# Performance work log

Hardware: AMD Instinct MI355X
Metric: run time of the kernel (lower is better)

## Reference

```python
import jax, jax.numpy as jnp
import numpy as np

EPS = 0.3
LAYERS = 2


def setup_inputs() -> dict:
    key = jax.random.key(0)
    ks = jax.random.split(key, 8)
    N, F, H, C, E = 50000, 512, 128, 40, 800000

    def xavier(k, shape):
        fan_out, fan_in = shape[0], shape[-1]
        std = 1.414 * np.sqrt(2.0 / (fan_in + fan_out))
        return (jax.random.normal(k, shape, jnp.float32) * std).astype(jnp.float32)

    return {
        "x": jax.random.normal(ks[0], (N, F), jnp.float32),
        "t1_w": xavier(ks[1], (H, F)),
        "t1_b": jnp.zeros((H,), jnp.float32),
        "t2_w": xavier(ks[2], (C, H)),
        "t2_b": jnp.zeros((C,), jnp.float32),
        "gate_w": xavier(ks[3], (LAYERS, 2 * H)),  # Linear(2H,1) weight per layer
        "gate_b": jnp.zeros((LAYERS,), jnp.float32),
        "edge_index": jax.random.randint(ks[4], (2, E), 0, N, jnp.int32),
    }


def reference(x, t1_w, t1_b, t2_w, t2_b, gate_w, gate_b, edge_index):
    N = x.shape[0]
    H = t1_w.shape[0]
    row, col = edge_index[0], edge_index[1]  # source, target

    # norm_degree = degree(row).clamp(min=1) ** -0.5
    deg = jax.ops.segment_sum(jnp.ones_like(row, dtype=x.dtype), row, num_segments=N)
    nd = jnp.clip(deg, 1.0) ** -0.5  # [N]
    nd_r, nd_c = nd[row], nd[col]    # [E]

    # dropout is identity in eval mode
    h = jax.nn.relu(x @ t1_w.T + t1_b)  # [N,H]
    raw = h
    for l in range(LAYERS):
        h_src = h[row]  # x_j, [E,H]
        h_dst = h[col]  # [E,H]
        # gate(cat([h[row], h[col]])) == h_src @ W[:H] + h_dst @ W[H:] + b
        g = jnp.tanh(h_src @ gate_w[l, :H] + h_dst @ gate_w[l, H:] + gate_b[l])  # [E]
        norm = g * nd_r * nd_c  # [E]
        agg = jax.ops.segment_sum(norm[:, None] * h_src, col, num_segments=N)  # scatter-add at targets
        h = EPS * raw + agg
    out = h @ t2_w.T + t2_b  # [N,C]
    return jax.nn.log_softmax(out, axis=1)
```

## Files before the change

kernel.cpp:

```cpp
#include <hip/hip_runtime.h>
#include <math.h>

#define F_DIM 512
#define H_DIM 128
#define C_DIM 40
#define EPS_F 0.3f
#define NBLK 256

typedef float f32x4 __attribute__((ext_vector_type(4)));
typedef unsigned int u32x4 __attribute__((ext_vector_type(4)));
typedef __bf16 bf16x8 __attribute__((ext_vector_type(8)));
typedef unsigned short ushort_t;
typedef unsigned char uchar_t;

__device__ inline float bflo(unsigned t) { return __builtin_bit_cast(float, t << 16); }
__device__ inline float bfhi(unsigned t) { return __builtin_bit_cast(float, t & 0xffff0000u); }
__device__ inline unsigned short f2bf(float f) {
  unsigned u = __builtin_bit_cast(unsigned, f);
  u = (u + 0x7fffu + ((u >> 16) & 1u)) >> 16;
  return (unsigned short)u;
}
__device__ inline unsigned pack2bf(float a, float b) {
  unsigned ua = __builtin_bit_cast(unsigned, a);
  unsigned ub = __builtin_bit_cast(unsigned, b);
  ua = (ua + 0x7fffu + ((ua >> 16) & 1u)) >> 16;
  ub = (ub + 0x7fffu + ((ub >> 16) & 1u)) >> 16;
  return ua | (ub << 16);
}


__global__ __launch_bounds__(256) void part_count(const int* __restrict__ row,
    const int* __restrict__ col, int* __restrict__ blkhist, int E, int nbkt, int chunk) {
  __shared__ int ch[256], rh[256];
  int t = threadIdx.x, b = blockIdx.x;
  ch[t] = 0; rh[t] = 0;
  __syncthreads();
  int s = b * chunk, e = min(E, s + chunk);
  for (int i = s + t; i < e; i += 256) {
    atomicAdd(&ch[((unsigned)col[i]) >> 8], 1);
    atomicAdd(&rh[((unsigned)row[i]) >> 8], 1);
  }
  __syncthreads();
  if (t < nbkt) {
    blkhist[t * NBLK + b] = ch[t];
    blkhist[(nbkt + t) * NBLK + b] = rh[t];
  }
}

__global__ __launch_bounds__(256) void part_scatter(const int* __restrict__ row,
    const int* __restrict__ col, const int* __restrict__ blkhist,
    int* __restrict__ bktbase, unsigned* __restrict__ colpart,
    uchar_t* __restrict__ rowpart, int E, int nbkt, int chunk) {
  __shared__ int sbase[400];
  __shared__ int stot[400];
  __shared__ int psum[256];
  __shared__ int sc[400];
  __shared__ int coff[400];
  int t = threadIdx.x, b = blockIdx.x;
  int nrows = 2 * nbkt;
  for (int rr = t; rr < nrows; rr += 256) {
    const int* rp = &blkhist[rr * NBLK];
    int pre = 0, tot = 0;
    for (int i = 0; i < NBLK; ++i) {
      int v = rp[i];
      pre += (i < b) ? v : 0;
      tot += v;
    }
    sbase[rr] = pre; stot[rr] = tot;
  }
  __syncthreads();
  int e0 = (2 * t     < nrows) ? stot[2 * t]     : 0;
  int e1 = (2 * t + 1 < nrows) ? stot[2 * t + 1] : 0;
  psum[t] = e0 + e1;
  __syncthreads();
  for (int off = 1; off < 256; off <<= 1) {
    int add = (t >= off) ? psum[t - off] : 0;
    __syncthreads();
    psum[t] += add;
    __syncthreads();
  }
  int pex = (t == 0) ? 0 : psum[t - 1];
  if (2 * t < nrows)     sc[2 * t]     = pex + sbase[2 * t];
  if (2 * t + 1 < nrows) sc[2 * t + 1] = pex + e0 + sbase[2 * t + 1];
  if (b == 0) {
    if (2 * t < nrows)     bktbase[2 * t]     = pex;
    if (2 * t + 1 < nrows) bktbase[2 * t + 1] = pex + e0;
    if (t == 0) bktbase[nrows] = 2 * E;
  }
  for (int rr = t; rr < nrows; rr += 256) coff[rr] = 0;
  __syncthreads();
  int s = b * chunk, e = min(E, s + chunk);
  for (int i = s + t; i < e; i += 256) {
    unsigned c = (unsigned)col[i], r = (unsigned)row[i];
    int bc = (int)(c >> 8), br = (int)(r >> 8);
    int pc = sc[bc] + atomicAdd(&coff[bc], 1);
    colpart[pc] = (r << 8) | (c & 255u);
    int pr = sc[nbkt + br] + atomicAdd(&coff[nbkt + br], 1) - E;
    rowpart[pr] = (uchar_t)(r & 255u);
  }
}

__global__ __launch_bounds__(256) void bucket_both(const unsigned* __restrict__ colpart,
    const uchar_t* __restrict__ rowpart, const int* __restrict__ bktbase,
    int* __restrict__ col_ptr, int* __restrict__ csr_src, float* __restrict__ nd,
    int N, int E, int nbkt) {
  __shared__ int cnt[256], ex[256], off[256];
  int t = threadIdx.x, bb = blockIdx.x;
  if (bb < nbkt) {
    int bkt = bb;
    int s = bktbase[bkt], e = bktbase[bkt + 1];
    cnt[t] = 0; off[t] = 0;
    __syncthreads();
    for (int i = s + t; i < e; i += 256)
      atomicAdd(&cnt[(int)(colpart[i] & 255u)], 1);
    __syncthreads();
    ex[t] = cnt[t];
    __syncthreads();
    for (int o = 1; o < 256; o <<= 1) {
      int v = (t >= o) ? ex[t - o] : 0;
      __syncthreads();
      ex[t] += v;
      __syncthreads();
    }
    int excl = (t == 0) ? 0 : ex[t - 1];
    __syncthreads();
    ex[t] = excl;
    __syncthreads();
    int node = bkt * 256 + t;
    if (node < N) col_ptr[node] = s + ex[t];
    if (bkt == 0 && t == 0) col_ptr[N] = E;
    for (int i = s + t; i < e; i += 256) {
      unsigned p = colpart[i];
      int lb = (int)(p & 255u);
      int dst = s + ex[lb] + atomicAdd(&off[lb], 1);
      csr_src[dst] = (int)(p >> 8);
    }
  } else {
    int bkt = bb - nbkt;
    int s = bktbase[nbkt + bkt] - E, e = bktbase[nbkt + bkt + 1] - E;
    cnt[t] = 0;
    __syncthreads();
    for (int i = s + t; i < e; i += 256)
      atomicAdd(&cnt[(int)rowpart[i]], 1);
    __syncthreads();
    int node = bkt * 256 + t;
    if (node < N) {
      int d = cnt[t] < 1 ? 1 : cnt[t];
      nd[node] = 1.0f / sqrtf((float)d);
    }
  }
}


__global__ __launch_bounds__(256) void gemm1_mfma(const float* __restrict__ x,
    const float* __restrict__ w, const float* __restrict__ b,
    ushort_t* __restrict__ hbf, int N) {
  __shared__ u32x4 AsBuf[1024];
  __shared__ u32x4 BsBuf[1024];
  char* Asc = (char*)AsBuf;
  char* Bsc = (char*)BsBuf;

  int t = threadIdx.x;
  int lane = t & 63;
  int wid = t >> 6;
  int wm = wid >> 1;
  int wn = wid & 1;
  int m0 = blockIdx.x * 128;

  f32x4 acc[4][4];
#pragma unroll
  for (int i = 0; i < 4; ++i)
#pragma unroll
    for (int j = 0; j < 4; ++j) acc[i][j] = (f32x4){0.f, 0.f, 0.f, 0.f};

  float bias[4];
#pragma unroll
  for (int j = 0; j < 4; ++j) bias[j] = b[wn * 64 + j * 16 + (lane & 15)];

  for (int kk = 0; kk < F_DIM; kk += 64) {
#pragma unroll
    for (int q = 0; q < 4; ++q) {
      int c = q * 256 + t;
      int row = c >> 3, kc = c & 7;
      int gm = m0 + row;
      f32x4 v0 = {0.f, 0.f, 0.f, 0.f}, v1 = {0.f, 0.f, 0.f, 0.f};
      if (gm < N) {
        const float* src = &x[(size_t)gm * F_DIM + kk + kc * 8];
        v0 = *(const f32x4*)src;
        v1 = *(const f32x4*)(src + 4);
      }
      u32x4 pk;
      pk[0] = pack2bf(v0[0], v0[1]);
      pk[1] = pack2bf(v0[2], v0[3]);
      pk[2] = pack2bf(v1[0], v1[1]);
      pk[3] = pack2bf(v1[2], v1[3]);
      *(u32x4*)(Asc + row * 128 + ((kc ^ (row & 7)) << 4)) = pk;
    }
#pragma unroll
    for (int q = 0; q < 4; ++q) {
      int c = q * 256 + t;
      int row = c >> 3, kc = c & 7;
      const float* src = &w[(size_t)row * F_DIM + kk + kc * 8];
      f32x4 v0 = *(const f32x4*)src;
      f32x4 v1 = *(const f32x4*)(src + 4);
      u32x4 pk;
      pk[0] = pack2bf(v0[0], v0[1]);
      pk[1] = pack2bf(v0[2], v0[3]);
      pk[2] = pack2bf(v1[0], v1[1]);
      pk[3] = pack2bf(v1[2], v1[3]);
      *(u32x4*)(Bsc + row * 128 + ((kc ^ (row & 7)) << 4)) = pk;
    }
    __syncthreads();
#pragma unroll
    for (int kh = 0; kh < 2; ++kh) {
      bf16x8 af[4], bfr[4];
      int kc = kh * 4 + (lane >> 4);
#pragma unroll
      for (int i = 0; i < 4; ++i) {
        int row = wm * 64 + i * 16 + (lane & 15);
        af[i] = *(const bf16x8*)(Asc + row * 128 + ((kc ^ (row & 7)) << 4));
      }
#pragma unroll
      for (int j = 0; j < 4; ++j) {
        int row = wn * 64 + j * 16 + (lane & 15);
        bfr[j] = *(const bf16x8*)(Bsc + row * 128 + ((kc ^ (row & 7)) << 4));
      }
#pragma unroll
      for (int i = 0; i < 4; ++i)
#pragma unroll
        for (int j = 0; j < 4; ++j)
          acc[i][j] = __builtin_amdgcn_mfma_f32_16x16x32_bf16(af[i], bfr[j], acc[i][j], 0, 0, 0);
    }
    __syncthreads();
  }

#pragma unroll
  for (int i = 0; i < 4; ++i)
#pragma unroll
    for (int j = 0; j < 4; ++j) {
      int col = wn * 64 + j * 16 + (lane & 15);
      int rbase = m0 + wm * 64 + i * 16 + ((lane >> 4) * 4);
#pragma unroll
      for (int r = 0; r < 4; ++r) {
        int gr = rbase + r;
        if (gr < N) hbf[(size_t)gr * H_DIM + col] = f2bf(fmaxf(acc[i][j][r] + bias[j], 0.f));
      }
    }
}


__global__ __launch_bounds__(256) void gate_s(const ushort_t* __restrict__ hbf,
    const float* __restrict__ gwl, const float* __restrict__ gb, int layer,
    float* __restrict__ s1, float* __restrict__ s2, int N) {
  int wid = (blockIdx.x * 256 + threadIdx.x) >> 6;
  int lane = threadIdx.x & 63;
  if (wid >= N) return;
  unsigned tv = *(const unsigned*)&hbf[(size_t)wid * H_DIM + lane * 2];
  float hx = bflo(tv), hy = bfhi(tv);
  float2 g1 = *(const float2*)&gwl[lane * 2];
  float2 g2 = *(const float2*)&gwl[H_DIM + lane * 2];
  float p1 = hx * g1.x + hy * g1.y;
  float p2 = hx * g2.x + hy * g2.y;
  for (int off = 32; off > 0; off >>= 1) {
    p1 += __shfl_xor(p1, off);
    p2 += __shfl_xor(p2, off);
  }
  if (lane == 0) {
    s1[wid] = p1;
    s2[wid] = p2 + gb[layer];
  }
}


template <bool GATE>
__global__ __launch_bounds__(256) void agg_kernel(const ushort_t* __restrict__ hbf,
    const ushort_t* __restrict__ rawbf, const float* __restrict__ s1,
    const float* __restrict__ s2pb, const float* __restrict__ nd,
    const int* __restrict__ col_ptr, const int* __restrict__ csr_src,
    ushort_t* __restrict__ houtbf,
    const float* __restrict__ gwl, const float* __restrict__ gb, int layer,
    float* __restrict__ s1o, float* __restrict__ s2o, int N) {
  int wid = (blockIdx.x * 256 + threadIdx.x) >> 6;
  int lane = threadIdx.x & 63;
  if (wid >= N) return;
  int v = wid;
  int p0 = col_ptr[v], p1 = col_ptr[v + 1];
  float s2v = s2pb[v];
  float ndv = nd[v];
  float ax = 0.f, ay = 0.f;
  for (int base = p0; base < p1; base += 64) {
    int idx = base + lane;
    int u = 0;
    float cf = 0.f;
    if (idx < p1) {
      u = csr_src[idx];
      cf = tanhf(s1[u] + s2v) * nd[u] * ndv;
    }
    int cnt = p1 - base;
    if (cnt > 64) cnt = 64;
    int j = 0;
    for (; j + 4 <= cnt; j += 4) {
      int u0 = __shfl(u, j + 0), u1 = __shfl(u, j + 1);
      int u2 = __shfl(u, j + 2), u3 = __shfl(u, j + 3);
      float c0 = __shfl(cf, j + 0), c1 = __shfl(cf, j + 1);
      float c2 = __shfl(cf, j + 2), c3 = __shfl(cf, j + 3);
      unsigned t0 = *(const unsigned*)&hbf[(size_t)u0 * H_DIM + lane * 2];
      unsigned t1 = *(const unsigned*)&hbf[(size_t)u1 * H_DIM + lane * 2];
      unsigned t2 = *(const unsigned*)&hbf[(size_t)u2 * H_DIM + lane * 2];
      unsigned t3 = *(const unsigned*)&hbf[(size_t)u3 * H_DIM + lane * 2];
      ax += c0 * bflo(t0) + c1 * bflo(t1) + c2 * bflo(t2) + c3 * bflo(t3);
      ay += c0 * bfhi(t0) + c1 * bfhi(t1) + c2 * bfhi(t2) + c3 * bfhi(t3);
    }
    for (; j < cnt; ++j) {
      int uj = __shfl(u, j);
      float cj = __shfl(cf, j);
      unsigned tj = *(const unsigned*)&hbf[(size_t)uj * H_DIM + lane * 2];
      ax += cj * bflo(tj);
      ay += cj * bfhi(tj);
    }
  }
  unsigned rv = *(const unsigned*)&rawbf[(size_t)v * H_DIM + lane * 2];
  float ox = EPS_F * bflo(rv) + ax;
  float oy = EPS_F * bfhi(rv) + ay;
  *(unsigned*)&houtbf[(size_t)v * H_DIM + lane * 2] = pack2bf(ox, oy);
  if (GATE) {
    float2 g1 = *(const float2*)&gwl[lane * 2];
    float2 g2 = *(const float2*)&gwl[H_DIM + lane * 2];
    float q1 = ox * g1.x + oy * g1.y;
    float q2 = ox * g2.x + oy * g2.y;
    for (int off = 32; off > 0; off >>= 1) {
      q1 += __shfl_xor(q1, off);
      q2 += __shfl_xor(q2, off);
    }
    if (lane == 0) {
      s1o[v] = q1;
      s2o[v] = q2 + gb[layer];
    }
  }
}


__global__ __launch_bounds__(256) void gemm2_lsm(const ushort_t* __restrict__ hbf,
    const float* __restrict__ w, const float* __restrict__ b,
    float* __restrict__ out, int N) {
  __shared__ float ws[C_DIM][129];
  __shared__ float bsh[C_DIM];
  __shared__ float hsm[4][H_DIM];
  int t = threadIdx.x;
  for (int i = t; i < C_DIM * H_DIM; i += 256) ws[i / H_DIM][i % H_DIM] = w[i];
  if (t < C_DIM) bsh[t] = b[t];
  __syncthreads();
  int wave = t >> 6, lane = t & 63;
  for (int vb = blockIdx.x * 4; vb < N; vb += gridDim.x * 4) {
    int v = vb + wave;
    bool act = v < N;
    if (act) {
      unsigned hv = *(const unsigned*)&hbf[(size_t)v * H_DIM + lane * 2];
      hsm[wave][lane * 2] = bflo(hv);
      hsm[wave][lane * 2 + 1] = bfhi(hv);
    }
    __syncthreads();
    float acc = 0.f;
    if (act && lane < C_DIM) {
#pragma unroll 8
      for (int k = 0; k < H_DIM; ++k)
        acc = fmaf(hsm[wave][k], ws[lane][k], acc);
      acc += bsh[lane];
    }
    float m = (lane < C_DIM) ? acc : -1e30f;
    for (int off = 32; off > 0; off >>= 1) m = fmaxf(m, __shfl_xor(m, off));
    float ex = (lane < C_DIM) ? expf(acc - m) : 0.f;
    float s = ex;
    for (int off = 32; off > 0; off >>= 1) s += __shfl_xor(s, off);
    float lse = m + logf(s);
    if (act && lane < C_DIM) out[(size_t)v * C_DIM + lane] = acc - lse;
    __syncthreads();
  }
}


extern "C" void kernel_launch(void* const* d_in, const int* in_sizes, int n_in,
                              void* d_out, int out_size, void* d_ws, size_t ws_size,
                              hipStream_t stream) {
  const float* x   = (const float*)d_in[0];
  const float* t1w = (const float*)d_in[1];
  const float* t1b = (const float*)d_in[2];
  const float* t2w = (const float*)d_in[3];
  const float* t2b = (const float*)d_in[4];
  const float* gw  = (const float*)d_in[5];
  const float* gb  = (const float*)d_in[6];
  const int*   ei  = (const int*)d_in[7];
  const int N = in_sizes[0] / F_DIM;
  const int E = in_sizes[7] / 2;
  float* out = (float*)d_out;

  char* p = (char*)d_ws;
  auto take = [&](size_t bytes) {
    char* r = p;
    p += (bytes + 255) & ~(size_t)255;
    return r;
  };
  ushort_t* h0 = (ushort_t*)take((size_t)N * H_DIM * 2);
  ushort_t* h1 = (ushort_t*)take((size_t)N * H_DIM * 2);
  ushort_t* h2 = (ushort_t*)take((size_t)N * H_DIM * 2);
  float* s1a = (float*)take((size_t)N * 4);
  float* s2a = (float*)take((size_t)N * 4);
  float* s1b = (float*)take((size_t)N * 4);
  float* s2b = (float*)take((size_t)N * 4);
  float* nd  = (float*)take((size_t)N * 4);
  int* col_ptr = (int*)take((size_t)(N + 1) * 4);
  int* csr_src = (int*)take((size_t)E * 4);

  const int nbkt = (N + 255) >> 8;
  const int chunk = (E + NBLK - 1) / NBLK;

  int* blkhist = (int*)take((size_t)2 * nbkt * NBLK * 4);
  int* bktbase = (int*)take((size_t)(2 * nbkt + 1) * 4);
  unsigned* colpart = (unsigned*)take((size_t)E * 4);
  uchar_t* rowpart  = (uchar_t*)take((size_t)E);

  const int* row = ei;
  const int* col = ei + E;

  gemm1_mfma<<<(N + 127) / 128, 256, 0, stream>>>(x, t1w, t1b, h0, N);

  part_count<<<NBLK, 256, 0, stream>>>(row, col, blkhist, E, nbkt, chunk);
  part_scatter<<<NBLK, 256, 0, stream>>>(row, col, blkhist, bktbase, colpart, rowpart, E, nbkt, chunk);
  bucket_both<<<2 * nbkt, 256, 0, stream>>>(colpart, rowpart, bktbase, col_ptr, csr_src, nd, N, E, nbkt);

  int nwb = (N + 3) / 4;
  gate_s<<<nwb, 256, 0, stream>>>(h0, gw + 0 * 2 * H_DIM, gb, 0, s1a, s2a, N);
  agg_kernel<true><<<nwb, 256, 0, stream>>>(h0, h0, s1a, s2a, nd, col_ptr, csr_src, h1,
                                            gw + 1 * 2 * H_DIM, gb, 1, s1b, s2b, N);
  agg_kernel<false><<<nwb, 256, 0, stream>>>(h1, h0, s1b, s2b, nd, col_ptr, csr_src, h2,
                                             nullptr, nullptr, 0, nullptr, nullptr, N);

  gemm2_lsm<<<1024, 256, 0, stream>>>(h2, t2w, t2b, out, N);
}
```

Baseline: 210.8 us.

## Fuse gate projection into GEMM1 and final GEMM/log-softmax into last aggregation

Computes the layer-0 gate dot products in the GEMM1 epilogue via cross-lane and shared-memory reductions, which removes the separate gate_s kernel and a reread of h0. The last aggregation now also does the output projection and log-softmax, so the h2 round trip and the gemm2 launch go away. Gate scores and the node degree norm are packed into one float2 per node to cut scattered gathers. The gather loop reads 16-byte chunks with four edges per wave iteration. In exchange, the final kernel loads the full output weight matrix into shared memory for every 4-node block, which may cost occupancy and time.

Result: faster. 192.6 us (-8.6%).

```diff
diff --git a/kernel.cpp b/kernel.cpp
--- a/kernel.cpp
+++ b/kernel.cpp
@@ -154,7 +154,10 @@
 
 __global__ __launch_bounds__(256) void gemm1_mfma(const float* __restrict__ x,
     const float* __restrict__ w, const float* __restrict__ b,
-    ushort_t* __restrict__ hbf, int N) {
+    const float* __restrict__ gwl, const float* __restrict__ gb,
+    const float* __restrict__ nd,
+    ushort_t* __restrict__ hbf, float2* __restrict__ pack0,
+    float* __restrict__ s2a, int N) {
   __shared__ u32x4 AsBuf[1024];
   __shared__ u32x4 BsBuf[1024];
   char* Asc = (char*)AsBuf;
@@ -166,6 +169,7 @@
   int wm = wid >> 1;
   int wn = wid & 1;
   int m0 = blockIdx.x * 128;
+  int ql = lane & 15;
 
   f32x4 acc[4][4];
 #pragma unroll
@@ -173,9 +177,14 @@
 #pragma unroll
     for (int j = 0; j < 4; ++j) acc[i][j] = (f32x4){0.f, 0.f, 0.f, 0.f};
 
-  float bias[4];
-#pragma unroll
-  for (int j = 0; j < 4; ++j) bias[j] = b[wn * 64 + j * 16 + (lane & 15)];
+  float bias[4], g1v[4], g2v[4];
+#pragma unroll
+  for (int j = 0; j < 4; ++j) {
+    int c = wn * 64 + j * 16 + ql;
+    bias[j] = b[c];
+    g1v[j] = gwl[c];
+    g2v[j] = gwl[H_DIM + c];
+  }
 
   for (int kk = 0; kk < F_DIM; kk += 64) {
 #pragma unroll
@@ -217,12 +226,12 @@
       int kc = kh * 4 + (lane >> 4);
 #pragma unroll
       for (int i = 0; i < 4; ++i) {
-        int row = wm * 64 + i * 16 + (lane & 15);
+        int row = wm * 64 + i * 16 + ql;
         af[i] = *(const bf16x8*)(Asc + row * 128 + ((kc ^ (row & 7)) << 4));
       }
 #pragma unroll
       for (int j = 0; j < 4; ++j) {
-        int row = wn * 64 + j * 16 + (lane & 15);
+        int row = wn * 64 + j * 16 + ql;
         bfr[j] = *(const bf16x8*)(Bsc + row * 128 + ((kc ^ (row & 7)) << 4));
       }
 #pragma unroll
@@ -234,147 +243,188 @@
     __syncthreads();
   }
 
+  float gp1[4][4], gp2[4][4];
 #pragma unroll
   for (int i = 0; i < 4; ++i)
 #pragma unroll
+    for (int r = 0; r < 4; ++r) { gp1[i][r] = 0.f; gp2[i][r] = 0.f; }
+
+#pragma unroll
+  for (int i = 0; i < 4; ++i) {
+    int rbase = m0 + wm * 64 + i * 16 + ((lane >> 4) * 4);
+#pragma unroll
     for (int j = 0; j < 4; ++j) {
-      int col = wn * 64 + j * 16 + (lane & 15);
-      int rbase = m0 + wm * 64 + i * 16 + ((lane >> 4) * 4);
+      int col = wn * 64 + j * 16 + ql;
 #pragma unroll
       for (int r = 0; r < 4; ++r) {
         int gr = rbase + r;
-        if (gr < N) hbf[(size_t)gr * H_DIM + col] = f2bf(fmaxf(acc[i][j][r] + bias[j], 0.f));
-      }
-    }
-}
-
-
-__global__ __launch_bounds__(256) void gate_s(const ushort_t* __restrict__ hbf,
-    const float* __restrict__ gwl, const float* __restrict__ gb, int layer,
-    float* __restrict__ s1, float* __restrict__ s2, int N) {
-  int wid = (blockIdx.x * 256 + threadIdx.x) >> 6;
-  int lane = threadIdx.x & 63;
-  if (wid >= N) return;
-  unsigned tv = *(const unsigned*)&hbf[(size_t)wid * H_DIM + lane * 2];
-  float hx = bflo(tv), hy = bfhi(tv);
-  float2 g1 = *(const float2*)&gwl[lane * 2];
-  float2 g2 = *(const float2*)&gwl[H_DIM + lane * 2];
-  float p1 = hx * g1.x + hy * g1.y;
-  float p2 = hx * g2.x + hy * g2.y;
-  for (int off = 32; off > 0; off >>= 1) {
-    p1 += __shfl_xor(p1, off);
-    p2 += __shfl_xor(p2, off);
-  }
-  if (lane == 0) {
-    s1[wid] = p1;
-    s2[wid] = p2 + gb[layer];
-  }
-}
-
-
-template <bool GATE>
+        float o = fmaxf(acc[i][j][r] + bias[j], 0.f);
+        if (gr < N) hbf[(size_t)gr * H_DIM + col] = f2bf(o);
+        gp1[i][r] = fmaf(o, g1v[j], gp1[i][r]);
+        gp2[i][r] = fmaf(o, g2v[j], gp2[i][r]);
+      }
+    }
+  }
+#pragma unroll
+  for (int i = 0; i < 4; ++i)
+#pragma unroll
+    for (int r = 0; r < 4; ++r) {
+#pragma unroll
+      for (int m = 1; m < 16; m <<= 1) {
+        gp1[i][r] += __shfl_xor(gp1[i][r], m);
+        gp2[i][r] += __shfl_xor(gp2[i][r], m);
+      }
+    }
+  float* pgA = (float*)AsBuf;
+  float* pgB = (float*)AsBuf + 256;
+  if (ql == 0) {
+#pragma unroll
+    for (int i = 0; i < 4; ++i)
+#pragma unroll
+      for (int r = 0; r < 4; ++r) {
+        int lr = wm * 64 + i * 16 + (lane >> 4) * 4 + r;
+        pgA[lr * 2 + wn] = gp1[i][r];
+        pgB[lr * 2 + wn] = gp2[i][r];
+      }
+  }
+  __syncthreads();
+  if (t < 128) {
+    int gr = m0 + t;
+    if (gr < N) {
+      float p1 = pgA[t * 2] + pgA[t * 2 + 1];
+      float p2 = pgB[t * 2] + pgB[t * 2 + 1];
+      float ndv = nd[gr];
+      pack0[gr] = make_float2(p1, ndv);
+      s2a[gr] = p2 + gb[0];
+    }
+  }
+}
+
+
+template <int MODE>
 __global__ __launch_bounds__(256) void agg_kernel(const ushort_t* __restrict__ hbf,
-    const ushort_t* __restrict__ rawbf, const float* __restrict__ s1,
+    const ushort_t* __restrict__ rawbf, const float2* __restrict__ pack,
     const float* __restrict__ s2pb, const float* __restrict__ nd,
     const int* __restrict__ col_ptr, const int* __restrict__ csr_src,
     ushort_t* __restrict__ houtbf,
-    const float* __restrict__ gwl, const float* __restrict__ gb, int layer,
-    float* __restrict__ s1o, float* __restrict__ s2o, int N) {
-  int wid = (blockIdx.x * 256 + threadIdx.x) >> 6;
-  int lane = threadIdx.x & 63;
-  if (wid >= N) return;
-  int v = wid;
-  int p0 = col_ptr[v], p1 = col_ptr[v + 1];
-  float s2v = s2pb[v];
-  float ndv = nd[v];
-  float ax = 0.f, ay = 0.f;
-  for (int base = p0; base < p1; base += 64) {
-    int idx = base + lane;
-    int u = 0;
-    float cf = 0.f;
-    if (idx < p1) {
-      u = csr_src[idx];
-      cf = tanhf(s1[u] + s2v) * nd[u] * ndv;
-    }
-    int cnt = p1 - base;
-    if (cnt > 64) cnt = 64;
-    int j = 0;
-    for (; j + 4 <= cnt; j += 4) {
-      int u0 = __shfl(u, j + 0), u1 = __shfl(u, j + 1);
-      int u2 = __shfl(u, j + 2), u3 = __shfl(u, j + 3);
-      float c0 = __shfl(cf, j + 0), c1 = __shfl(cf, j + 1);
-      float c2 = __shfl(cf, j + 2), c3 = __shfl(cf, j + 3);
-      unsigned t0 = *(const unsigned*)&hbf[(size_t)u0 * H_DIM + lane * 2];
-      unsigned t1 = *(const unsigned*)&hbf[(size_t)u1 * H_DIM + lane * 2];
-      unsigned t2 = *(const unsigned*)&hbf[(size_t)u2 * H_DIM + lane * 2];
-      unsigned t3 = *(const unsigned*)&hbf[(size_t)u3 * H_DIM + lane * 2];
-      ax += c0 * bflo(t0) + c1 * bflo(t1) + c2 * bflo(t2) + c3 * bflo(t3);
-      ay += c0 * bfhi(t0) + c1 * bfhi(t1) + c2 * bfhi(t2) + c3 * bfhi(t3);
-    }
-    for (; j < cnt; ++j) {
-      int uj = __shfl(u, j);
-      float cj = __shfl(cf, j);
-      unsigned tj = *(const unsigned*)&hbf[(size_t)uj * H_DIM + lane * 2];
-      ax += cj * bflo(tj);
-      ay += cj * bfhi(tj);
-    }
-  }
-  unsigned rv = *(const unsigned*)&rawbf[(size_t)v * H_DIM + lane * 2];
-  float ox = EPS_F * bflo(rv) + ax;
-  float oy = EPS_F * bfhi(rv) + ay;
-  *(unsigned*)&houtbf[(size_t)v * H_DIM + lane * 2] = pack2bf(ox, oy);
-  if (GATE) {
-    float2 g1 = *(const float2*)&gwl[lane * 2];
-    float2 g2 = *(const float2*)&gwl[H_DIM + lane * 2];
-    float q1 = ox * g1.x + oy * g1.y;
-    float q2 = ox * g2.x + oy * g2.y;
-    for (int off = 32; off > 0; off >>= 1) {
-      q1 += __shfl_xor(q1, off);
-      q2 += __shfl_xor(q2, off);
-    }
-    if (lane == 0) {
-      s1o[v] = q1;
-      s2o[v] = q2 + gb[layer];
-    }
-  }
-}
-
-
-__global__ __launch_bounds__(256) void gemm2_lsm(const ushort_t* __restrict__ hbf,
-    const float* __restrict__ w, const float* __restrict__ b,
+    const float* __restrict__ gwl, const float* __restrict__ gb,
+    float2* __restrict__ packo, float* __restrict__ s2o,
+    const float* __restrict__ w2, const float* __restrict__ b2,
     float* __restrict__ out, int N) {
-  __shared__ float ws[C_DIM][129];
-  __shared__ float bsh[C_DIM];
-  __shared__ float hsm[4][H_DIM];
+  __shared__ float ws[(MODE == 2 ? C_DIM : 1)][129];
+  __shared__ float bsh[(MODE == 2 ? C_DIM : 1)];
+  __shared__ float hsm[(MODE == 2 ? 4 : 1)][H_DIM];
   int t = threadIdx.x;
-  for (int i = t; i < C_DIM * H_DIM; i += 256) ws[i / H_DIM][i % H_DIM] = w[i];
-  if (t < C_DIM) bsh[t] = b[t];
-  __syncthreads();
   int wave = t >> 6, lane = t & 63;
-  for (int vb = blockIdx.x * 4; vb < N; vb += gridDim.x * 4) {
-    int v = vb + wave;
-    bool act = v < N;
-    if (act) {
-      unsigned hv = *(const unsigned*)&hbf[(size_t)v * H_DIM + lane * 2];
-      hsm[wave][lane * 2] = bflo(hv);
-      hsm[wave][lane * 2 + 1] = bfhi(hv);
-    }
-    __syncthreads();
-    float acc = 0.f;
+  int g = lane >> 4, q = lane & 15;
+  if (MODE == 2) {
+    for (int i = t; i < C_DIM * H_DIM; i += 256) ws[i / H_DIM][i % H_DIM] = w2[i];
+    if (t < C_DIM) bsh[t] = b2[t];
+    __syncthreads();
+  }
+  int v = blockIdx.x * 4 + wave;
+  bool act = v < N;
+
+  float acc8[8];
+#pragma unroll
+  for (int k = 0; k < 8; ++k) acc8[k] = 0.f;
+  float o[8];
+  float ndv = 0.f;
+
+  if (act) {
+    int p0 = col_ptr[v], p1 = col_ptr[v + 1];
+    float s2v = s2pb[v];
+    ndv = nd[v];
+    for (int base = p0; base < p1; base += 64) {
+      int idx = base + lane;
+      int u = 0;
+      float cf = 0.f;
+      if (idx < p1) {
+        u = csr_src[idx];
+        float2 pk = pack[u];
+        cf = tanhf(pk.x + s2v) * pk.y * ndv;
+      }
+      int cnt = p1 - base;
+      if (cnt > 64) cnt = 64;
+      for (int j = 0; j < cnt; j += 4) {
+        int e = j + g;
+        int ue = __shfl(u, e);
+        float ce = __shfl(cf, e);
+        u32x4 hv = *(const u32x4*)&hbf[(size_t)ue * H_DIM + q * 8];
+        acc8[0] = fmaf(ce, bflo(hv[0]), acc8[0]);
+        acc8[1] = fmaf(ce, bfhi(hv[0]), acc8[1]);
+        acc8[2] = fmaf(ce, bflo(hv[1]), acc8[2]);
+        acc8[3] = fmaf(ce, bfhi(hv[1]), acc8[3]);
+        acc8[4] = fmaf(ce, bflo(hv[2]), acc8[4]);
+        acc8[5] = fmaf(ce, bfhi(hv[2]), acc8[5]);
+        acc8[6] = fmaf(ce, bflo(hv[3]), acc8[6]);
+        acc8[7] = fmaf(ce, bfhi(hv[3]), acc8[7]);
+      }
+    }
+#pragma unroll
+    for (int k = 0; k < 8; ++k) {
+      acc8[k] += __shfl_xor(acc8[k], 16);
+      acc8[k] += __shfl_xor(acc8[k], 32);
+    }
+    u32x4 rv = *(const u32x4*)&rawbf[(size_t)v * H_DIM + q * 8];
+    o[0] = fmaf(EPS_F, bflo(rv[0]), acc8[0]);
+    o[1] = fmaf(EPS_F, bfhi(rv[0]), acc8[1]);
+    o[2] = fmaf(EPS_F, bflo(rv[1]), acc8[2]);
+    o[3] = fmaf(EPS_F, bfhi(rv[1]), acc8[3]);
+    o[4] = fmaf(EPS_F, bflo(rv[2]), acc8[4]);
+    o[5] = fmaf(EPS_F, bfhi(rv[2]), acc8[5]);
+    o[6] = fmaf(EPS_F, bflo(rv[3]), acc8[6]);
+    o[7] = fmaf(EPS_F, bfhi(rv[3]), acc8[7]);
+
+    if (MODE == 1) {
+      if (g == 0) {
+        u32x4 pk;
+        pk[0] = pack2bf(o[0], o[1]);
+        pk[1] = pack2bf(o[2], o[3]);
+        pk[2] = pack2bf(o[4], o[5]);
+        pk[3] = pack2bf(o[6], o[7]);
+        *(u32x4*)&houtbf[(size_t)v * H_DIM + q * 8] = pk;
+      }
+      f32x4 ga0 = *(const f32x4*)&gwl[q * 8];
+      f32x4 ga1 = *(const f32x4*)&gwl[q * 8 + 4];
+      f32x4 gb0 = *(const f32x4*)&gwl[H_DIM + q * 8];
+      f32x4 gb1 = *(const f32x4*)&gwl[H_DIM + q * 8 + 4];
+      float q1 = o[0] * ga0[0] + o[1] * ga0[1] + o[2] * ga0[2] + o[3] * ga0[3]
+               + o[4] * ga1[0] + o[5] * ga1[1] + o[6] * ga1[2] + o[7] * ga1[3];
+      float q2 = o[0] * gb0[0] + o[1] * gb0[1] + o[2] * gb0[2] + o[3] * gb0[3]
+               + o[4] * gb1[0] + o[5] * gb1[1] + o[6] * gb1[2] + o[7] * gb1[3];
+#pragma unroll
+      for (int m = 1; m < 16; m <<= 1) {
+        q1 += __shfl_xor(q1, m);
+        q2 += __shfl_xor(q2, m);
+      }
+      if (lane == 0) {
+        packo[v] = make_float2(q1, ndv);
+        s2o[v] = q2 + gb[0];
+      }
+    }
+  }
+
+  if (MODE == 2) {
+    if (act && g == 0) {
+#pragma unroll
+      for (int k = 0; k < 8; ++k) hsm[wave][q * 8 + k] = o[k];
+    }
+    __syncthreads();
+    float accv = 0.f;
     if (act && lane < C_DIM) {
 #pragma unroll 8
       for (int k = 0; k < H_DIM; ++k)
-        acc = fmaf(hsm[wave][k], ws[lane][k], acc);
-      acc += bsh[lane];
-    }
-    float m = (lane < C_DIM) ? acc : -1e30f;
+        accv = fmaf(hsm[wave][k], ws[lane][k], accv);
+      accv += bsh[lane];
+    }
+    float m = (lane < C_DIM) ? accv : -1e30f;
     for (int off = 32; off > 0; off >>= 1) m = fmaxf(m, __shfl_xor(m, off));
-    float ex = (lane < C_DIM) ? expf(acc - m) : 0.f;
+    float ex = (lane < C_DIM) ? expf(accv - m) : 0.f;
     float s = ex;
     for (int off = 32; off > 0; off >>= 1) s += __shfl_xor(s, off);
     float lse = m + logf(s);
-    if (act && lane < C_DIM) out[(size_t)v * C_DIM + lane] = acc - lse;
-    __syncthreads();
+    if (act && lane < C_DIM) out[(size_t)v * C_DIM + lane] = accv - lse;
   }
 }
 
@@ -402,10 +452,9 @@
   };
   ushort_t* h0 = (ushort_t*)take((size_t)N * H_DIM * 2);
   ushort_t* h1 = (ushort_t*)take((size_t)N * H_DIM * 2);
-  ushort_t* h2 = (ushort_t*)take((size_t)N * H_DIM * 2);
-  float* s1a = (float*)take((size_t)N * 4);
+  float2* pack0 = (float2*)take((size_t)N * 8);
+  float2* pack1 = (float2*)take((size_t)N * 8);
   float* s2a = (float*)take((size_t)N * 4);
-  float* s1b = (float*)take((size_t)N * 4);
   float* s2b = (float*)take((size_t)N * 4);
   float* nd  = (float*)take((size_t)N * 4);
   int* col_ptr = (int*)take((size_t)(N + 1) * 4);
@@ -422,18 +471,17 @@
   const int* row = ei;
   const int* col = ei + E;
 
-  gemm1_mfma<<<(N + 127) / 128, 256, 0, stream>>>(x, t1w, t1b, h0, N);
-
   part_count<<<NBLK, 256, 0, stream>>>(row, col, blkhist, E, nbkt, chunk);
   part_scatter<<<NBLK, 256, 0, stream>>>(row, col, blkhist, bktbase, colpart, rowpart, E, nbkt, chunk);
   bucket_both<<<2 * nbkt, 256, 0, stream>>>(colpart, rowpart, bktbase, col_ptr, csr_src, nd, N, E, nbkt);
 
+  gemm1_mfma<<<(N + 127) / 128, 256, 0, stream>>>(x, t1w, t1b, gw, gb, nd, h0, pack0, s2a, N);
+
   int nwb = (N + 3) / 4;
-  gate_s<<<nwb, 256, 0, stream>>>(h0, gw + 0 * 2 * H_DIM, gb, 0, s1a, s2a, N);
-  agg_kernel<true><<<nwb, 256, 0, stream>>>(h0, h0, s1a, s2a, nd, col_ptr, csr_src, h1,
-                                            gw + 1 * 2 * H_DIM, gb, 1, s1b, s2b, N);
-  agg_kernel<false><<<nwb, 256, 0, stream>>>(h1, h0, s1b, s2b, nd, col_ptr, csr_src, h2,
-                                             nullptr, nullptr, 0, nullptr, nullptr, N);
-
-  gemm2_lsm<<<1024, 256, 0, stream>>>(h2, t2w, t2b, out, N);
-}
+  agg_kernel<1><<<nwb, 256, 0, stream>>>(h0, h0, pack0, s2a, nd, col_ptr, csr_src, h1,
+                                         gw + 2 * H_DIM, gb + 1, pack1, s2b,
+                                         nullptr, nullptr, nullptr, N);
+  agg_kernel<2><<<nwb, 256, 0, stream>>>(h1, h0, pack1, s2b, nd, col_ptr, csr_src, nullptr,
+                                         nullptr, nullptr, nullptr, nullptr,
+                                         t2w, t2b, out, N);
+}
```
